# Performance work log

Hardware: AMD Instinct MI355X
Metric: run time of the kernel (lower is better)

## Reference

```python
import jax, jax.numpy as jnp
import numpy as np

N_NODES = 20000
DIM = 128
N_EDGES = 500000
BATCH = 16384
EPS = 1e-6  # torch.nn.PairwiseDistance default eps


def setup_inputs() -> dict:
    key = jax.random.key(0)
    k = jax.random.split(key, 8)
    edges = jax.random.randint(k[0], (2, N_EDGES), 0, N_NODES, dtype=jnp.int64 if jax.config.jax_enable_x64 else jnp.int32)
    nodes_p_star = jnp.sort(jax.random.randint(k[1], (BATCH,), 0, N_NODES))
    nodes_p = jnp.sort(jax.random.randint(k[2], (BATCH,), 0, N_NODES))
    # learned parameters, init in [-1, 1) as in the torch module
    beta_p = 2.0 * jax.random.uniform(k[3], (N_NODES,), dtype=jnp.float32) - 1.0
    beta_p_star = 2.0 * jax.random.uniform(k[4], (N_NODES,), dtype=jnp.float32) - 1.0
    p = 2.0 * jax.random.uniform(k[5], (N_NODES, DIM), dtype=jnp.float32) - 1.0
    p_star = 2.0 * jax.random.uniform(k[6], (N_NODES, DIM), dtype=jnp.float32) - 1.0
    return {
        "edges": edges,
        "nodes_p_star": nodes_p_star,
        "nodes_p": nodes_p,
        "beta_p": beta_p,
        "beta_p_star": beta_p_star,
        "p": p,
        "p_star": p_star,
    }


def reference(edges, nodes_p_star, nodes_p, beta_p, beta_p_star, p, p_star):
    # ---- link term: sum over observed edges of (beta - dist) ----
    beta_pair = beta_p_star[edges[0]] + beta_p[edges[1]]  # [E]
    diff = p[edges[0]] - p_star[edges[1]]                 # [E, D]
    # torch PairwiseDistance adds eps to the difference before the norm
    z_dist = jnp.sqrt(jnp.sum((diff + EPS) ** 2, axis=-1))
    link_term = jnp.sum(beta_pair - z_dist)

    # ---- non-link term: triu-masked sum of exp(beta - cdist) ----
    bps = beta_p_star[nodes_p_star]   # [Ns]
    bp = beta_p[nodes_p]              # [Np]
    ps = p_star[nodes_p_star]         # [Ns, D]
    pp = p[nodes_p]                   # [Np, D]
    beta_mat = bps[None, :] + bp[:, None]          # [Np, Ns]
    # cdist(ps, pp) -> [Ns, Np] via Gram trick
    sq = (jnp.sum(ps * ps, axis=-1)[:, None]
          + jnp.sum(pp * pp, axis=-1)[None, :]
          - 2.0 * jnp.einsum('nd,md->nm', ps, pp))
    dist_mat = jnp.sqrt(jnp.maximum(sq, 0.0))      # [Ns, Np]
    intensity = jnp.exp(beta_mat.T - dist_mat)     # [Ns, Np]
    non_link = jnp.sum(jnp.triu(intensity, k=1))

    return -(link_term - non_link)
```

## Files before the change

kernel.cpp:

```cpp
#include <hip/hip_runtime.h>
#include <hip/hip_bf16.h>
#include <hip/hip_fp8.h>

#define N_NODES 20000
#define DIM 128
#define N_EDGES 500000
#define BATCH 16384
#define EPS 1e-6f
#define L2E 1.4426950408889634f

typedef float f32x4 __attribute__((ext_vector_type(4)));
typedef float f32x2 __attribute__((ext_vector_type(2)));
typedef long long i64_t;

__device__ __forceinline__ float fast_sqrtf(float x) {
#if __has_builtin(__builtin_amdgcn_sqrtf)
    return __builtin_amdgcn_sqrtf(x);
#else
    return sqrtf(x);
#endif
}
__device__ __forceinline__ float fast_exp2f(float x) {
#if __has_builtin(__builtin_amdgcn_exp2f)
    return __builtin_amdgcn_exp2f(x);
#else
    return exp2f(x);
#endif
}
__device__ __forceinline__ f32x2 splat2(float s) { f32x2 r = {s, s}; return r; }
__device__ __forceinline__ f32x2 max2(f32x2 a, f32x2 b) {
#if __has_builtin(__builtin_elementwise_max)
    return __builtin_elementwise_max(a, b);
#else
    f32x2 r; r.x = fmaxf(a.x, b.x); r.y = fmaxf(a.y, b.y); return r;
#endif
}

__device__ __forceinline__ unsigned pack4_fp8(float a, float b, float c, float d) {
#if __has_builtin(__builtin_amdgcn_cvt_pk_fp8_f32)
    unsigned v = 0;
    v = __builtin_amdgcn_cvt_pk_fp8_f32(a, b, v, false);
    v = __builtin_amdgcn_cvt_pk_fp8_f32(c, d, v, true);
    return v;
#else
    __hip_fp8_e4m3 x0(a), x1(b), x2(c), x3(d);
    return (unsigned)x0.__x | ((unsigned)x1.__x << 8) |
           ((unsigned)x2.__x << 16) | ((unsigned)x3.__x << 24);
#endif
}

template <bool HI>
__device__ __forceinline__ f32x2 unpack2_fp8(unsigned v) {
#if __has_builtin(__builtin_amdgcn_cvt_pk_f32_fp8)
    return __builtin_amdgcn_cvt_pk_f32_fp8((int)v, HI);
#else
    __hip_fp8_e4m3 t0, t1;
    t0.__x = (unsigned char)(HI ? (v >> 16) : v);
    t1.__x = (unsigned char)(HI ? (v >> 24) : (v >> 8));
    f32x2 r; r.x = (float)t0; r.y = (float)t1;
    return r;
#endif
}

#define OFF_N2A   0
#define OFF_N2B   65536
#define OFF_BA    131072
#define OFF_BB    196608
#define OFF_A8    262144
#define OFF_B8    2359296
#define OFF_P8    4456448
#define OFF_PS8   7016448
#define OFF_N2PT  9576448
#define OFF_N2PST 9656448
#define OFF_BTP   9736448
#define OFF_BTPS  9816448
#define OFF_END   9896448

__global__ __launch_bounds__(256) void prep1_kernel(
    const float* __restrict__ p, const float* __restrict__ ps,
    const float* __restrict__ beta_p, const float* __restrict__ beta_ps,
    unsigned char* __restrict__ p8, unsigned char* __restrict__ ps8,
    float* __restrict__ n2pt, float* __restrict__ n2pst,
    float* __restrict__ btp, float* __restrict__ btps,
    float* __restrict__ out)
{
    const int b = blockIdx.x;
    if (b == 0 && threadIdx.x == 0) out[0] = 0.f;
    if (b < 5000) {
        const bool isP = b < 2500;
        const float* src = isP ? p : ps;
        unsigned char* dst = isP ? p8 : ps8;
        float* n2t = isP ? n2pt : n2pst;
        const int g = threadIdx.x & 31;
        const int row = (isP ? b : b - 2500) * 8 + (threadIdx.x >> 5);
        float4 v = ((const float4*)(src + (size_t)row * DIM))[g];
        ((unsigned*)(dst + (size_t)row * DIM))[g] = pack4_fp8(v.x, v.y, v.z, v.w);
        float nrm = v.x * v.x + v.y * v.y + v.z * v.z + v.w * v.w;
        #pragma unroll
        for (int m = 16; m >= 1; m >>= 1) nrm += __shfl_xor(nrm, m, 32);
        if (g == 0) n2t[row] = nrm;
    } else {
        int t = (b - 5000) * 256 + threadIdx.x;
        if (t < N_NODES) btp[t] = L2E * beta_p[t];
        else if (t < 2 * N_NODES) btps[t - N_NODES] = L2E * beta_ps[t - N_NODES];
    }
}

__global__ __launch_bounds__(256) void prep2_kernel(
    const int* __restrict__ nodes_ps, const int* __restrict__ nodes_p,
    const unsigned char* __restrict__ p8, const unsigned char* __restrict__ ps8,
    const float* __restrict__ n2pt, const float* __restrict__ n2pst,
    const float* __restrict__ btp, const float* __restrict__ btps,
    unsigned char* __restrict__ A8, float* __restrict__ n2A, float* __restrict__ bA2,
    unsigned char* __restrict__ B8, float* __restrict__ n2B, float* __restrict__ bB2)
{
    const int b = blockIdx.x;
    const bool isA = b < 512;
    const int row = (isA ? b : b - 512) * 32 + (threadIdx.x >> 3);
    const int l8 = threadIdx.x & 7;
    const int id = isA ? nodes_ps[row] : nodes_p[row];
    const unsigned char* tbl = isA ? ps8 : p8;
    unsigned char* dst = isA ? A8 : B8;
    uint4 v = *(const uint4*)(tbl + (size_t)id * DIM + l8 * 16);
    *(uint4*)(dst + (size_t)row * DIM + l8 * 16) = v;
    if (l8 == 0) {
        if (isA) { n2A[row] = n2pst[id]; bA2[row] = btps[id]; }
        else     { n2B[row] = n2pt[id];  bB2[row] = btp[id]; }
    }
}

#define LSTRIDE 144
__global__ __launch_bounds__(512, 4) void main_kernel(
    const unsigned char* __restrict__ Ag, const unsigned char* __restrict__ Bg,
    const float* __restrict__ n2A, const float* __restrict__ n2B,
    const float* __restrict__ bA2, const float* __restrict__ bB2,
    const int* __restrict__ edges,
    const float* __restrict__ beta_p, const float* __restrict__ beta_ps,
    const unsigned char* __restrict__ p8, const unsigned char* __restrict__ ps8,
    float* __restrict__ out)
{
    const int bx = blockIdx.x, by = blockIdx.y;
    int ti, tj;
    const int len = 128 - by;
    if (bx < len) { ti = by; tj = by + bx; }
    else          { ti = 127 - by; tj = 127 - (bx - len); }
    const int i0 = ti * 128, j0 = tj * 128;
    const int bid = by * 129 + bx;
    const bool diag = (ti == tj);

    __shared__ __align__(16) unsigned char As[128 * LSTRIDE];
    __shared__ __align__(16) unsigned char Bs[128 * LSTRIDE];
    __shared__ float smr[8];

    const int tid = threadIdx.x;
    const int lane = tid & 63;
    const int w = tid >> 6;
    const int wm = w & 3;
    const int wn = w >> 2;
    const int quad = lane >> 4;
    const int lr = lane & 15;

    const int le = bid * 64 + w * 8 + (lane >> 3);
    const int lch = lane & 7;
    const bool ev = (le < N_EDGES);
    int e0 = 0, e1 = 0;
    float ebeta = 0.f;
    if (ev) {
        e0 = edges[le];
        e1 = edges[N_EDGES + le];
        if (lch == 0) ebeta = beta_ps[e0] + beta_p[e1];
    }

    #pragma unroll
    for (int c = tid; c < 1024; c += 512) {
        int row = c >> 3, col = (c & 7) * 16;
        *(uint4*)&As[row * LSTRIDE + col] = *(const uint4*)(Ag + (size_t)(i0 + row) * DIM + col);
        *(uint4*)&Bs[row * LSTRIDE + col] = *(const uint4*)(Bg + (size_t)(j0 + row) * DIM + col);
    }
    __syncthreads();

    uint4 ua = {0,0,0,0}, ub = {0,0,0,0};
    if (ev) {
        ua = *(const uint4*)(p8 + (size_t)e0 * DIM + lch * 16);
        ub = *(const uint4*)(ps8 + (size_t)e1 * DIM + lch * 16);
    }
    const int ilo = i0 + wm * 32, jlo = j0 + wn * 64;
    float4 n2i[2], bi[2];
    #pragma unroll
    for (int mi = 0; mi < 2; ++mi) {
        n2i[mi] = *(const float4*)&n2A[ilo + mi * 16 + quad * 4];
        bi[mi]  = *(const float4*)&bA2[ilo + mi * 16 + quad * 4];
    }
    float n2j[4], bj[4];
    #pragma unroll
    for (int ni = 0; ni < 4; ++ni) {
        n2j[ni] = n2B[jlo + ni * 16 + lr];
        bj[ni]  = bB2[jlo + ni * 16 + lr];
    }

    int cls = 0;
    if (diag) cls = (wn == 0) ? (wm >= 2 ? 2 : 1) : (wm >= 2 ? 1 : 0);

    float lsum = 0.f;
    f32x2 lsum2 = {0.f, 0.f};
    if (cls != 2) {
        f32x4 acc[2][4] = {};
        #pragma unroll
        for (int ks = 0; ks < 4; ++ks) {
            int koff = ks * 32 + quad * 8;
            i64_t af[2], bf[4];
            #pragma unroll
            for (int u = 0; u < 2; ++u)
                af[u] = *(const i64_t*)&As[(wm * 32 + u * 16 + lr) * LSTRIDE + koff];
            #pragma unroll
            for (int v = 0; v < 4; ++v)
                bf[v] = *(const i64_t*)&Bs[(wn * 64 + v * 16 + lr) * LSTRIDE + koff];
            #pragma unroll
            for (int mi = 0; mi < 2; ++mi)
                #pragma unroll
                for (int ni = 0; ni < 4; ++ni)
                    acc[mi][ni] = __builtin_amdgcn_mfma_f32_16x16x32_fp8_fp8(af[mi], bf[ni], acc[mi][ni], 0, 0, 0);
        }

        if (cls == 0) {
            #pragma unroll
            for (int mi = 0; mi < 2; ++mi) {
                f32x2 n2iA = {n2i[mi].x, n2i[mi].y}, n2iB = {n2i[mi].z, n2i[mi].w};
                f32x2 biA  = {bi[mi].x,  bi[mi].y},  biB  = {bi[mi].z,  bi[mi].w};
                #pragma unroll
                for (int ni = 0; ni < 4; ++ni) {
                    f32x4 d = acc[mi][ni];
                    f32x2 d0 = {d[0], d[1]}, d1 = {d[2], d[3]};
                    f32x2 bsum0 = biA + splat2(bj[ni]);
                    f32x2 bsum1 = biB + splat2(bj[ni]);
                    f32x2 sq0 = max2(d0 * splat2(-2.f) + (n2iA + splat2(n2j[ni])), splat2(0.f));
                    f32x2 sq1 = max2(d1 * splat2(-2.f) + (n2iB + splat2(n2j[ni])), splat2(0.f));
                    f32x2 dist0 = {fast_sqrtf(sq0.x), fast_sqrtf(sq0.y)};
                    f32x2 dist1 = {fast_sqrtf(sq1.x), fast_sqrtf(sq1.y)};
                    f32x2 arg0 = dist0 * splat2(-L2E) + bsum0;
                    f32x2 arg1 = dist1 * splat2(-L2E) + bsum1;
                    f32x2 ex0 = {fast_exp2f(arg0.x), fast_exp2f(arg0.y)};
                    f32x2 ex1 = {fast_exp2f(arg1.x), fast_exp2f(arg1.y)};
                    lsum2 += ex0 + ex1;
                }
            }
        } else {
            #pragma unroll
            for (int mi = 0; mi < 2; ++mi)
                #pragma unroll
                for (int ni = 0; ni < 4; ++ni) {
                    f32x4 d = acc[mi][ni];
                    #pragma unroll
                    for (int r = 0; r < 4; ++r) {
                        int ig = ilo + mi * 16 + quad * 4 + r;
                        int jg = jlo + ni * 16 + lr;
                        float tt = ((const float*)&n2i[mi])[r] + n2j[ni];
                        float sq = fmaxf(fmaf(d[r], -2.f, tt), 0.f);
                        float arg = fmaf(fast_sqrtf(sq), -L2E, ((const float*)&bi[mi])[r] + bj[ni]);
                        float ex = fast_exp2f(arg);
                        if (jg > ig) lsum += ex;
                    }
                }
        }
    }
    lsum += lsum2.x + lsum2.y;

    if (ev) {
        float s = 0.f;
        #pragma unroll
        for (int d = 0; d < 4; ++d) {
            unsigned va = ((const unsigned*)&ua)[d];
            unsigned vb = ((const unsigned*)&ub)[d];
            f32x2 a0 = unpack2_fp8<false>(va), a1 = unpack2_fp8<true>(va);
            f32x2 b0 = unpack2_fp8<false>(vb), b1 = unpack2_fp8<true>(vb);
            float t0 = a0.x - b0.x + EPS, t1 = a0.y - b0.y + EPS;
            float t2 = a1.x - b1.x + EPS, t3 = a1.y - b1.y + EPS;
            s = fmaf(t0, t0, s); s = fmaf(t1, t1, s);
            s = fmaf(t2, t2, s); s = fmaf(t3, t3, s);
        }
        #pragma unroll
        for (int m = 4; m >= 1; m >>= 1) s += __shfl_xor(s, m, 8);
        if (lch == 0) lsum -= ebeta - fast_sqrtf(s);
    }

    #pragma unroll
    for (int m = 32; m >= 1; m >>= 1) lsum += __shfl_xor(lsum, m, 64);
    if (lane == 0) smr[w] = lsum;
    __syncthreads();
    if (tid == 0) {
        float t = 0.f;
        #pragma unroll
        for (int i = 0; i < 8; ++i) t += smr[i];
        atomicAdd(out, t);
    }
}

extern "C" void kernel_launch(void* const* d_in, const int* in_sizes, int n_in,
                              void* d_out, int out_size, void* d_ws, size_t ws_size,
                              hipStream_t stream) {
    const int* edges = (const int*)d_in[0];
    const int* nodes_p_star = (const int*)d_in[1];
    const int* nodes_p = (const int*)d_in[2];
    const float* beta_p = (const float*)d_in[3];
    const float* beta_p_star = (const float*)d_in[4];
    const float* p = (const float*)d_in[5];
    const float* p_star = (const float*)d_in[6];

    char* ws = (char*)d_ws;
    float* n2A = (float*)(ws + OFF_N2A);
    float* n2B = (float*)(ws + OFF_N2B);
    float* bA2 = (float*)(ws + OFF_BA);
    float* bB2 = (float*)(ws + OFF_BB);
    unsigned char* A8 = (unsigned char*)(ws + OFF_A8);
    unsigned char* B8 = (unsigned char*)(ws + OFF_B8);
    unsigned char* p8 = (unsigned char*)(ws + OFF_P8);
    unsigned char* ps8 = (unsigned char*)(ws + OFF_PS8);
    float* n2pt = (float*)(ws + OFF_N2PT);
    float* n2pst = (float*)(ws + OFF_N2PST);
    float* btp = (float*)(ws + OFF_BTP);
    float* btps = (float*)(ws + OFF_BTPS);

    prep1_kernel<<<5157, 256, 0, stream>>>(
        p, p_star, beta_p, beta_p_star, p8, ps8, n2pt, n2pst, btp, btps, (float*)d_out);

    prep2_kernel<<<1024, 256, 0, stream>>>(
        nodes_p_star, nodes_p, p8, ps8, n2pt, n2pst, btp, btps,
        A8, n2A, bA2, B8, n2B, bB2);

    main_kernel<<<dim3(129, 64), 512, 0, stream>>>(
        A8, B8, n2A, n2B, bA2, bB2,
        edges, beta_p, beta_p_star, p8, ps8, (float*)d_out);
}
```

Before: 198.7 us.

## Load MFMA fragments directly from global memory with register double-buffering

Removes the shared-memory staging of the A/B fp8 tiles and the block-wide barrier. Each wave now loads its MFMA operand fragments straight from global memory (L2-resident packed arrays), prefetching the next k-step into a second register buffer. The epilogue's norm and bias loads move after the MFMA loop to shorten live ranges, and the packed epilogue math is reshuffled into scalar fmax/fma. The cost is redundant, uncoalesced 8-byte global loads, since several waves share the same rows.

```diff
diff --git a/kernel.cpp b/kernel.cpp
--- a/kernel.cpp
+++ b/kernel.cpp
@@ -25,14 +25,6 @@
     return __builtin_amdgcn_exp2f(x);
 #else
     return exp2f(x);
-#endif
-}
-__device__ __forceinline__ f32x2 splat2(float s) { f32x2 r = {s, s}; return r; }
-__device__ __forceinline__ f32x2 max2(f32x2 a, f32x2 b) {
-#if __has_builtin(__builtin_elementwise_max)
-    return __builtin_elementwise_max(a, b);
-#else
-    f32x2 r; r.x = fmaxf(a.x, b.x); r.y = fmaxf(a.y, b.y); return r;
 #endif
 }
 
@@ -129,7 +121,6 @@
     }
 }
 
-#define LSTRIDE 144
 __global__ __launch_bounds__(512, 4) void main_kernel(
     const unsigned char* __restrict__ Ag, const unsigned char* __restrict__ Bg,
     const float* __restrict__ n2A, const float* __restrict__ n2B,
@@ -148,8 +139,6 @@
     const int bid = by * 129 + bx;
     const bool diag = (ti == tj);
 
-    __shared__ __align__(16) unsigned char As[128 * LSTRIDE];
-    __shared__ __align__(16) unsigned char Bs[128 * LSTRIDE];
     __shared__ float smr[8];
 
     const int tid = threadIdx.x;
@@ -165,38 +154,16 @@
     const bool ev = (le < N_EDGES);
     int e0 = 0, e1 = 0;
     float ebeta = 0.f;
+    uint4 ua = {0,0,0,0}, ub = {0,0,0,0};
     if (ev) {
         e0 = edges[le];
         e1 = edges[N_EDGES + le];
-        if (lch == 0) ebeta = beta_ps[e0] + beta_p[e1];
-    }
-
-    #pragma unroll
-    for (int c = tid; c < 1024; c += 512) {
-        int row = c >> 3, col = (c & 7) * 16;
-        *(uint4*)&As[row * LSTRIDE + col] = *(const uint4*)(Ag + (size_t)(i0 + row) * DIM + col);
-        *(uint4*)&Bs[row * LSTRIDE + col] = *(const uint4*)(Bg + (size_t)(j0 + row) * DIM + col);
-    }
-    __syncthreads();
-
-    uint4 ua = {0,0,0,0}, ub = {0,0,0,0};
-    if (ev) {
         ua = *(const uint4*)(p8 + (size_t)e0 * DIM + lch * 16);
         ub = *(const uint4*)(ps8 + (size_t)e1 * DIM + lch * 16);
-    }
+        if (lch == 0) ebeta = beta_ps[e0] + beta_p[e1];
+    }
+
     const int ilo = i0 + wm * 32, jlo = j0 + wn * 64;
-    float4 n2i[2], bi[2];
-    #pragma unroll
-    for (int mi = 0; mi < 2; ++mi) {
-        n2i[mi] = *(const float4*)&n2A[ilo + mi * 16 + quad * 4];
-        bi[mi]  = *(const float4*)&bA2[ilo + mi * 16 + quad * 4];
-    }
-    float n2j[4], bj[4];
-    #pragma unroll
-    for (int ni = 0; ni < 4; ++ni) {
-        n2j[ni] = n2B[jlo + ni * 16 + lr];
-        bj[ni]  = bB2[jlo + ni * 16 + lr];
-    }
 
     int cls = 0;
     if (diag) cls = (wn == 0) ? (wm >= 2 ? 2 : 1) : (wm >= 2 ? 1 : 0);
@@ -204,22 +171,44 @@
     float lsum = 0.f;
     f32x2 lsum2 = {0.f, 0.f};
     if (cls != 2) {
+        const unsigned char* Abase = Ag + (size_t)(ilo + lr) * DIM + quad * 8;
+        const unsigned char* Bbase = Bg + (size_t)(jlo + lr) * DIM + quad * 8;
+
+        i64_t af[2][2], bf[2][4];
+        #pragma unroll
+        for (int u = 0; u < 2; ++u) af[0][u] = *(const i64_t*)(Abase + u * 16 * DIM);
+        #pragma unroll
+        for (int v = 0; v < 4; ++v) bf[0][v] = *(const i64_t*)(Bbase + v * 16 * DIM);
+
         f32x4 acc[2][4] = {};
         #pragma unroll
         for (int ks = 0; ks < 4; ++ks) {
-            int koff = ks * 32 + quad * 8;
-            i64_t af[2], bf[4];
-            #pragma unroll
-            for (int u = 0; u < 2; ++u)
-                af[u] = *(const i64_t*)&As[(wm * 32 + u * 16 + lr) * LSTRIDE + koff];
-            #pragma unroll
-            for (int v = 0; v < 4; ++v)
-                bf[v] = *(const i64_t*)&Bs[(wn * 64 + v * 16 + lr) * LSTRIDE + koff];
+            const int cur = ks & 1, nxt = cur ^ 1;
+            if (ks < 3) {
+                const int ko = (ks + 1) * 32;
+                #pragma unroll
+                for (int u = 0; u < 2; ++u) af[nxt][u] = *(const i64_t*)(Abase + u * 16 * DIM + ko);
+                #pragma unroll
+                for (int v = 0; v < 4; ++v) bf[nxt][v] = *(const i64_t*)(Bbase + v * 16 * DIM + ko);
+            }
             #pragma unroll
             for (int mi = 0; mi < 2; ++mi)
                 #pragma unroll
                 for (int ni = 0; ni < 4; ++ni)
-                    acc[mi][ni] = __builtin_amdgcn_mfma_f32_16x16x32_fp8_fp8(af[mi], bf[ni], acc[mi][ni], 0, 0, 0);
+                    acc[mi][ni] = __builtin_amdgcn_mfma_f32_16x16x32_fp8_fp8(af[cur][mi], bf[cur][ni], acc[mi][ni], 0, 0, 0);
+        }
+
+        float4 n2i[2], bi[2];
+        #pragma unroll
+        for (int mi = 0; mi < 2; ++mi) {
+            n2i[mi] = *(const float4*)&n2A[ilo + mi * 16 + quad * 4];
+            bi[mi]  = *(const float4*)&bA2[ilo + mi * 16 + quad * 4];
+        }
+        float n2j[4], bj[4];
+        #pragma unroll
+        for (int ni = 0; ni < 4; ++ni) {
+            n2j[ni] = n2B[jlo + ni * 16 + lr];
+            bj[ni]  = bB2[jlo + ni * 16 + lr];
         }
 
         if (cls == 0) {
@@ -231,17 +220,18 @@
                 for (int ni = 0; ni < 4; ++ni) {
                     f32x4 d = acc[mi][ni];
                     f32x2 d0 = {d[0], d[1]}, d1 = {d[2], d[3]};
-                    f32x2 bsum0 = biA + splat2(bj[ni]);
-                    f32x2 bsum1 = biB + splat2(bj[ni]);
-                    f32x2 sq0 = max2(d0 * splat2(-2.f) + (n2iA + splat2(n2j[ni])), splat2(0.f));
-                    f32x2 sq1 = max2(d1 * splat2(-2.f) + (n2iB + splat2(n2j[ni])), splat2(0.f));
-                    f32x2 dist0 = {fast_sqrtf(sq0.x), fast_sqrtf(sq0.y)};
-                    f32x2 dist1 = {fast_sqrtf(sq1.x), fast_sqrtf(sq1.y)};
-                    f32x2 arg0 = dist0 * splat2(-L2E) + bsum0;
-                    f32x2 arg1 = dist1 * splat2(-L2E) + bsum1;
-                    f32x2 ex0 = {fast_exp2f(arg0.x), fast_exp2f(arg0.y)};
-                    f32x2 ex1 = {fast_exp2f(arg1.x), fast_exp2f(arg1.y)};
-                    lsum2 += ex0 + ex1;
+                    f32x2 nj = {n2j[ni], n2j[ni]};
+                    f32x2 bb = {bj[ni], bj[ni]};
+                    f32x2 sq0 = d0 * (f32x2){-2.f, -2.f} + (n2iA + nj);
+                    f32x2 sq1 = d1 * (f32x2){-2.f, -2.f} + (n2iB + nj);
+                    sq0.x = fmaxf(sq0.x, 0.f); sq0.y = fmaxf(sq0.y, 0.f);
+                    sq1.x = fmaxf(sq1.x, 0.f); sq1.y = fmaxf(sq1.y, 0.f);
+                    f32x2 arg0 = {fmaf(fast_sqrtf(sq0.x), -L2E, biA.x + bb.x),
+                                  fmaf(fast_sqrtf(sq0.y), -L2E, biA.y + bb.y)};
+                    f32x2 arg1 = {fmaf(fast_sqrtf(sq1.x), -L2E, biB.x + bb.x),
+                                  fmaf(fast_sqrtf(sq1.y), -L2E, biB.y + bb.y)};
+                    lsum2 += (f32x2){fast_exp2f(arg0.x), fast_exp2f(arg0.y)};
+                    lsum2 += (f32x2){fast_exp2f(arg1.x), fast_exp2f(arg1.y)};
                 }
             }
         } else {
```

Result: slower. 289.1 us (+45.5%).
